# Kernel optimization log

Measured on AMD Instinct MI355X. Metric: run time of the kernel, lower is better.

Reference implementation:

```python
import jax, jax.numpy as jnp
import numpy as np

B, L, F = 256, 512, 64
NUM_IDS = 2000
LN_EPS = 1e-5


def setup_inputs() -> dict:
    key = jax.random.key(0)
    ks = jax.random.split(key, 16)
    s = 0.05
    return {
        # padded neighbor-id sequences; 0 is the padding id
        "src_ids": jax.random.randint(ks[0], (B, L), 0, NUM_IDS, dtype=jnp.int64)
        if jax.config.jax_enable_x64 else jax.random.randint(ks[0], (B, L), 0, NUM_IDS, dtype=jnp.int32),
        "dst_ids": jax.random.randint(ks[1], (B, L), 0, NUM_IDS, dtype=jnp.int64)
        if jax.config.jax_enable_x64 else jax.random.randint(ks[1], (B, L), 0, NUM_IDS, dtype=jnp.int32),
        # co-occurrence encode MLP: Linear(1->F), ReLU, Linear(F->F)
        "enc_w1": jax.random.normal(ks[2], (1, F), jnp.float32) * s,
        "enc_b1": jax.random.normal(ks[3], (F,), jnp.float32) * s,
        "enc_w2": jax.random.normal(ks[4], (F, F), jnp.float32) * s,
        "enc_b2": jax.random.normal(ks[5], (F,), jnp.float32) * s,
        # cross-attention projections (bias-free q/k/v as in source)
        "Wq": jax.random.normal(ks[6], (F, F), jnp.float32) * s,
        "Wk": jax.random.normal(ks[7], (F, F), jnp.float32) * s,
        "Wv": jax.random.normal(ks[8], (F, F), jnp.float32) * s,
        "Wo": jax.random.normal(ks[9], (F, F), jnp.float32) * s,
        "bo": jax.random.normal(ks[10], (F,), jnp.float32) * s,
        "ln_g": jnp.ones((F,), jnp.float32),
        "ln_b": jnp.zeros((F,), jnp.float32),
    }


def _counts_in(a, b):
    # for each element of a: how many times does it occur in b (same batch row)
    # equivalent to the np.unique count / mapping-dict lookup in the original
    return (a[:, :, None] == b[:, None, :]).sum(axis=-1).astype(jnp.float32)


def _appearances(a, b):
    # [B, L, 2]: counts of each id of `a` in (a, b); zero out padding (id==0)
    app = jnp.stack([_counts_in(a, a), _counts_in(a, b)], axis=-1)
    return jnp.where((a == 0)[..., None], 0.0, app)


def _encode(app, w1, b1, w2, b2):
    # Linear(1->F) -> ReLU -> Linear(F->F), then sum over the 2 count channels
    h = jax.nn.relu(app[..., None] * w1[0] + b1)  # [B, L, 2, F]
    h = jnp.einsum('blcf,fg->blcg', h, w2) + b2
    return h.sum(axis=2)  # [B, L, F]


def _linear_attn(q, k, v):
    dim = q.shape[-1]
    q = jax.nn.softmax(q, axis=-1) * (dim ** -0.5)
    k = jax.nn.softmax(k, axis=1)  # softmax over sequence dim (dim=-2)
    ctx = jnp.einsum('bld,ble->bde', k, v)
    return jnp.einsum('bld,bde->ble', q, ctx)


def _layer_norm(x, g, b):
    mu = x.mean(axis=-1, keepdims=True)
    var = ((x - mu) ** 2).mean(axis=-1, keepdims=True)
    return (x - mu) * jax.lax.rsqrt(var + LN_EPS) * g + b


def _cross_attn(x, ctx, Wq, Wk, Wv, Wo, bo, ln_g, ln_b):
    q, k, v = x @ Wq, ctx @ Wk, ctx @ Wv
    attn = _linear_attn(q, k, v)
    return _layer_norm(x + attn @ Wo + bo, ln_g, ln_b)


def reference(src_ids, dst_ids, enc_w1, enc_b1, enc_w2, enc_b2,
              Wq, Wk, Wv, Wo, bo, ln_g, ln_b):
    # neighbor co-occurrence counting + encoding
    src_app = _appearances(src_ids, dst_ids)  # [B, L, 2]
    dst_app = _appearances(dst_ids, src_ids)
    src_feat = _encode(src_app, enc_w1, enc_b1, enc_w2, enc_b2)  # [B, L, F]
    dst_feat = _encode(dst_app, enc_w1, enc_b1, enc_w2, enc_b2)
    # linear cross-attention fusion (shared weights, both directions)
    src_out = _cross_attn(src_feat, dst_feat, Wq, Wk, Wv, Wo, bo, ln_g, ln_b)
    dst_out = _cross_attn(dst_feat, src_feat, Wq, Wk, Wv, Wo, bo, ln_g, ln_b)
    return jnp.stack([src_out, dst_out])  # [2, B, L, F]
```

## Files before the change

### kernel.cpp

```cpp
#include <hip/hip_runtime.h>
#include <hip/hip_bf16.h>

#define BB 256
#define LL 512
#define NIDS 2000

typedef float nfloat4 __attribute__((ext_vector_type(4)));

#define WS_TABLE 0

__global__ __launch_bounds__(64) void k_table(
    const float* __restrict__ w1, const float* __restrict__ b1,
    const float* __restrict__ w2, const float* __restrict__ b2,
    float* __restrict__ table) {
  int c = blockIdx.x, f = threadIdx.x;
  __shared__ float h[64];
  h[f] = fmaxf((float)c * w1[f] + b1[f], 0.f);
  __syncthreads();
  float acc = b2[f];
#pragma unroll
  for (int g = 0; g < 64; ++g) acc += h[g] * w2[g * 64 + f];
  table[c * 64 + f] = acc;
}

__global__ __launch_bounds__(256, 3) void k_fused(
    const int* __restrict__ src, const int* __restrict__ dst,
    const float* __restrict__ table,
    const float* __restrict__ Wq, const float* __restrict__ Wk,
    const float* __restrict__ Wv, const float* __restrict__ Wo,
    const float* __restrict__ bo, const float* __restrict__ lng,
    const float* __restrict__ lnb, float* __restrict__ out) {
  __shared__ __align__(16) char smem[50192];
  int*   hist  = (int*)smem;
  float* poolF = (float*)smem;
  int*   hkey  = (int*)(smem + 16384);
  int*   hmult = (int*)(smem + 20480);
  float* fbF   = (float*)(smem + 20480);
  float* Mg    = (float*)(smem + 24576);
  int*   xkey  = (int*)(smem + 41984);
  int*   ckey  = (int*)(smem + 44032);
  int*   cmult = (int*)(smem + 46080);
  int*   pidxl = (int*)(smem + 48128);
  int*   npp   = (int*)(smem + 50176);

  int bd = blockIdx.x, b = bd >> 1, dir = bd & 1;
  int tid = threadIdx.x, tx = tid & 63, ty = tid >> 6;
  int e0 = ty * 16;

  const int* s = src + b * LL;
  const int* d = dst + b * LL;
  int sid0 = s[tid], sid1 = s[tid + 256];
  int did0 = d[tid], did1 = d[tid + 256];
  for (int i = tid; i < 4000; i += 256) hist[i] = 0;
  __syncthreads();
  atomicAdd(&hist[sid0], 1);        atomicAdd(&hist[sid1], 1);
  atomicAdd(&hist[2000 + did0], 1); atomicAdd(&hist[2000 + did1], 1);
  __syncthreads();

  int x0 = dir ? did0 : sid0, x1 = dir ? did1 : sid1;
  int c0 = dir ? sid0 : did0, c1 = dir ? sid1 : did1;
  const int* hx = dir ? hist + 2000 : hist;
  const int* hc = dir ? hist : hist + 2000;

  for (int i = tid; i < 1024; i += 256) { hkey[i] = -1; hmult[i] = 0; }
  if (tid == 0) *npp = 0;
  __syncthreads();
  for (int r = 0; r < 2; ++r) {
    int id = r ? c1 : c0;
    int ca = 0, cb = 0;
    if (id != 0) { ca = hc[id]; cb = hx[id]; }
    int key = ca | (cb << 10);
    int h = (int)(((unsigned)key * 2654435761u) >> 22) & 1023;
    while (true) {
      int old = atomicCAS(&hkey[h], -1, key);
      if (old == -1 || old == key) break;
      h = (h + 1) & 1023;
    }
    atomicAdd(&hmult[h], 1);
  }
  __syncthreads();
  for (int i = tid; i < 1024; i += 256) {
    if (hkey[i] != -1) {
      int idx = atomicAdd(npp, 1);
      ckey[idx]  = hkey[i];
      cmult[idx] = hmult[i];
    }
  }
  __syncthreads();
  int Pc = *npp;
  __syncthreads();

  for (int i = tid; i < 1024; i += 256) { hkey[i] = -1; hmult[i] = 0; }
  if (tid == 0) *npp = 0;
  __syncthreads();
  int slot0, slot1;
  for (int r = 0; r < 2; ++r) {
    int id = r ? x1 : x0;
    int ca = 0, cb = 0;
    if (id != 0) { ca = hx[id]; cb = hc[id]; }
    int key = ca | (cb << 10);
    int h = (int)(((unsigned)key * 2654435761u) >> 22) & 1023;
    while (true) {
      int old = atomicCAS(&hkey[h], -1, key);
      if (old == -1 || old == key) break;
      h = (h + 1) & 1023;
    }
    if (r) slot1 = h; else slot0 = h;
  }
  __syncthreads();
  for (int i = tid; i < 1024; i += 256) {
    int k = hkey[i];
    if (k != -1) {
      int idx = atomicAdd(npp, 1);
      xkey[idx] = k;
      hkey[i] = idx;
    }
  }
  __syncthreads();
  pidxl[tid]       = hkey[slot0];
  pidxl[tid + 256] = hkey[slot1];
  int Px = *npp;
  __syncthreads();

  float* featA = poolF;
  float* pA    = poolF + 1024;
  float* vA    = poolF + 2048;
  float wa[64];
  float macc[16];
#pragma unroll
  for (int e = 0; e < 16; ++e) macc[e] = 0.f;
  float sacc = 0.f;

  for (int j0 = 0; j0 < Pc; j0 += 16) {
    int cN = min(16, Pc - j0);
#pragma unroll
    for (int f = 0; f < 64; ++f) wa[f] = Wk[f * 64 + tx];
    for (int j = ty; j < cN; j += 4) {
      int key = ckey[j0 + j];
      int ca = key & 1023, cb = key >> 10;
      featA[j * 64 + tx] = table[ca * 64 + tx] + table[cb * 64 + tx];
      float kr = 0.f;
      const float4* fb4 = (const float4*)&featA[j * 64];
#pragma unroll
      for (int q = 0; q < 16; ++q) {
        float4 fv = fb4[q];
        kr += fv.x * wa[4 * q] + fv.y * wa[4 * q + 1] + fv.z * wa[4 * q + 2] + fv.w * wa[4 * q + 3];
      }
      float p = __expf(kr) * (float)cmult[j0 + j];
      sacc += p;
      pA[j * 64 + tx] = p;
    }
#pragma unroll
    for (int f = 0; f < 64; ++f) wa[f] = Wv[f * 64 + tx];
    for (int j = ty; j < cN; j += 4) {
      float vr = 0.f;
      const float4* fb4 = (const float4*)&featA[j * 64];
#pragma unroll
      for (int q = 0; q < 16; ++q) {
        float4 fv = fb4[q];
        vr += fv.x * wa[4 * q] + fv.y * wa[4 * q + 1] + fv.z * wa[4 * q + 2] + fv.w * wa[4 * q + 3];
      }
      vA[j * 64 + tx] = vr;
    }
    __syncthreads();
    for (int jj = 0; jj < cN; ++jj) {
      float pg = pA[jj * 64 + tx];
      const float4* vb4 = (const float4*)&vA[jj * 64 + e0];
#pragma unroll
      for (int q = 0; q < 4; ++q) {
        float4 vv = vb4[q];
        macc[4 * q]     += pg * vv.x; macc[4 * q + 1] += pg * vv.y;
        macc[4 * q + 2] += pg * vv.z; macc[4 * q + 3] += pg * vv.w;
      }
    }
    __syncthreads();
  }
  fbF[512 + ty * 64 + tx] = sacc;
  __syncthreads();
  float inv = 1.f / (fbF[512 + tx] + fbF[576 + tx] + fbF[640 + tx] + fbF[704 + tx]);
#pragma unroll
  for (int e = 0; e < 16; ++e) Mg[(e0 + e) * 68 + tx] = macc[e] * inv;
  for (int i = tid; i < 4096; i += 256) poolF[i] = Wo[i];
#pragma unroll
  for (int f = 0; f < 64; ++f) wa[f] = Wq[f * 64 + tx];
  float bov = bo[tx], lg = lng[tx], lb = lnb[tx];
  __syncthreads();

#pragma unroll
  for (int e = 0; e < 16; ++e) macc[e] = 0.f;
  for (int f = 0; f < 64; ++f) {
    float mt = Mg[f * 68 + tx];
    const float4* wo4 = (const float4*)&poolF[f * 64 + e0];
#pragma unroll
    for (int q = 0; q < 4; ++q) {
      float4 w4 = wo4[q];
      macc[4 * q]     += mt * w4.x; macc[4 * q + 1] += mt * w4.y;
      macc[4 * q + 2] += mt * w4.z; macc[4 * q + 3] += mt * w4.w;
    }
  }
  __syncthreads();
#pragma unroll
  for (int e = 0; e < 16; ++e) Mg[(e0 + e) * 68 + tx] = macc[e];
  __syncthreads();

  for (int i0 = 0; i0 < Px; i0 += 64) {
    int cN = min(64, Px - i0);
    for (int jj = ty; jj < cN; jj += 4) {
      int key = xkey[i0 + jj];
      int ca = key & 1023, cb = key >> 10;
      float fv = table[ca * 64 + tx] + table[cb * 64 + tx];
      fbF[ty * 64 + tx] = fv;
      float qr = 0.f;
      const float4* fb4 = (const float4*)&fbF[ty * 64];
#pragma unroll
      for (int q = 0; q < 16; ++q) {
        float4 f4v = fb4[q];
        qr += f4v.x * wa[4 * q] + f4v.y * wa[4 * q + 1] + f4v.z * wa[4 * q + 2] + f4v.w * wa[4 * q + 3];
      }
      float p = __expf(qr);
      float sum = p;
#pragma unroll
      for (int off = 32; off >= 1; off >>= 1) sum += __shfl_xor(sum, off, 64);
      float qh = p / sum * 0.125f;
      fbF[256 + ty * 64 + tx] = qh;
      float at = 0.f;
      const float4* qb4 = (const float4*)&fbF[256 + ty * 64];
      const float4* gt4 = (const float4*)&Mg[tx * 68];
#pragma unroll
      for (int q = 0; q < 16; ++q) {
        float4 qv = qb4[q];
        float4 gv = gt4[q];
        at += qv.x * gv.x + qv.y * gv.y + qv.z * gv.z + qv.w * gv.w;
      }
      float r = fv + at + bov;
      float mu = r;
#pragma unroll
      for (int off = 32; off >= 1; off >>= 1) mu += __shfl_xor(mu, off, 64);
      mu *= (1.f / 64.f);
      float dv = r - mu;
      float var = dv * dv;
#pragma unroll
      for (int off = 32; off >= 1; off >>= 1) var += __shfl_xor(var, off, 64);
      var *= (1.f / 64.f);
      poolF[jj * 64 + tx] = dv * rsqrtf(var + 1e-5f) * lg + lb;
    }
    __syncthreads();
    const nfloat4* w4 = (const nfloat4*)poolF;
    nfloat4* out4 = (nfloat4*)(out + (size_t)(dir * BB + b) * (LL * 64));
    for (int idx = tid; idx < 512 * 16; idx += 256) {
      int l = idx >> 4, q = idx & 15;
      int pid = pidxl[l];
      if (pid >= i0 && pid < i0 + cN)
        __builtin_nontemporal_store(w4[(pid - i0) * 16 + q], &out4[l * 16 + q]);
    }
    __syncthreads();
  }
}

extern "C" void kernel_launch(void* const* d_in, const int* in_sizes, int n_in,
                              void* d_out, int out_size, void* d_ws, size_t ws_size,
                              hipStream_t stream) {
  const int* src  = (const int*)d_in[0];
  const int* dst  = (const int*)d_in[1];
  const float* w1 = (const float*)d_in[2];
  const float* b1 = (const float*)d_in[3];
  const float* w2 = (const float*)d_in[4];
  const float* b2 = (const float*)d_in[5];
  const float* Wq = (const float*)d_in[6];
  const float* Wk = (const float*)d_in[7];
  const float* Wv = (const float*)d_in[8];
  const float* Wo = (const float*)d_in[9];
  const float* bo = (const float*)d_in[10];
  const float* lng = (const float*)d_in[11];
  const float* lnb = (const float*)d_in[12];
  float* out = (float*)d_out;
  float* table = (float*)d_ws + WS_TABLE;

  k_table<<<dim3(513), dim3(64), 0, stream>>>(w1, b1, w2, b2, table);
  k_fused<<<dim3(512), dim3(256), 0, stream>>>(src, dst, table,
                                               Wq, Wk, Wv, Wo, bo, lng, lnb, out);
}
```

Baseline: 129.8 us.

## Fuse encode-table computation into main kernel with per-block compacted LDS table

Drops the separate k_table launch. Each block now collects the distinct count values used by its keys, computes encoded feature rows only for those values into shared memory, and remaps keys to local indices. Feature gathers then read LDS instead of a global table, and one kernel launch is saved. In exchange each block redoes the MLP work for its own values, and shared memory grows to about 76KB with occupancy lowered to 2 blocks.

```diff
diff --git a/kernel.cpp b/kernel.cpp
--- a/kernel.cpp
+++ b/kernel.cpp
@@ -3,45 +3,32 @@
 
 #define BB 256
 #define LL 512
-#define NIDS 2000
 
 typedef float nfloat4 __attribute__((ext_vector_type(4)));
 
-#define WS_TABLE 0
-
-__global__ __launch_bounds__(64) void k_table(
+__global__ __launch_bounds__(256, 2) void k_all(
+    const int* __restrict__ src, const int* __restrict__ dst,
     const float* __restrict__ w1, const float* __restrict__ b1,
     const float* __restrict__ w2, const float* __restrict__ b2,
-    float* __restrict__ table) {
-  int c = blockIdx.x, f = threadIdx.x;
-  __shared__ float h[64];
-  h[f] = fmaxf((float)c * w1[f] + b1[f], 0.f);
-  __syncthreads();
-  float acc = b2[f];
-#pragma unroll
-  for (int g = 0; g < 64; ++g) acc += h[g] * w2[g * 64 + f];
-  table[c * 64 + f] = acc;
-}
-
-__global__ __launch_bounds__(256, 3) void k_fused(
-    const int* __restrict__ src, const int* __restrict__ dst,
-    const float* __restrict__ table,
     const float* __restrict__ Wq, const float* __restrict__ Wk,
     const float* __restrict__ Wv, const float* __restrict__ Wo,
     const float* __restrict__ bo, const float* __restrict__ lng,
     const float* __restrict__ lnb, float* __restrict__ out) {
-  __shared__ __align__(16) char smem[50192];
+  __shared__ __align__(16) char smem[77840];
   int*   hist  = (int*)smem;
   float* poolF = (float*)smem;
   int*   hkey  = (int*)(smem + 16384);
   int*   hmult = (int*)(smem + 20480);
-  float* fbF   = (float*)(smem + 20480);
-  float* Mg    = (float*)(smem + 24576);
-  int*   xkey  = (int*)(smem + 41984);
-  int*   ckey  = (int*)(smem + 44032);
-  int*   cmult = (int*)(smem + 46080);
-  int*   pidxl = (int*)(smem + 48128);
-  int*   npp   = (int*)(smem + 50176);
+  float* tabL  = (float*)(smem + 16384);
+  int*   cflag = (int*)(smem + 49152);
+  int*   clist = (int*)(smem + 51252);
+  float* Mg    = (float*)(smem + 49152);
+  int*   xkey  = (int*)(smem + 66560);
+  int*   ckey  = (int*)(smem + 68608);
+  int*   cmult = (int*)(smem + 70656);
+  int*   pidxl = (int*)(smem + 72704);
+  float* fbF   = (float*)(smem + 74752);
+  int*   npp   = (int*)(smem + 77824);
 
   int bd = blockIdx.x, b = bd >> 1, dir = bd & 1;
   int tid = threadIdx.x, tx = tid & 63, ty = tid >> 6;
@@ -90,7 +77,7 @@
   int Pc = *npp;
   __syncthreads();
 
-  for (int i = tid; i < 1024; i += 256) { hkey[i] = -1; hmult[i] = 0; }
+  for (int i = tid; i < 1024; i += 256) { hkey[i] = -1; }
   if (tid == 0) *npp = 0;
   __syncthreads();
   int slot0, slot1;
@@ -122,10 +109,48 @@
   int Px = *npp;
   __syncthreads();
 
+  for (int i = tid; i < 513; i += 256) cflag[i] = 0;
+  if (tid == 0) *npp = 0;
+  __syncthreads();
+  if (tid < Pc) { int k = ckey[tid]; cflag[k & 1023] = 1; cflag[k >> 10] = 1; }
+  if (tid < Px) { int k = xkey[tid]; cflag[k & 1023] = 1; cflag[k >> 10] = 1; }
+  __syncthreads();
+  for (int c = tid; c < 513; c += 256) {
+    if (cflag[c]) {
+      int idx = atomicAdd(npp, 1);
+      clist[idx] = c;
+      cflag[c] = idx;
+    }
+  }
+  __syncthreads();
+  int nc = *npp;
+  if (tid < Pc) { int k = ckey[tid]; ckey[tid] = cflag[k & 1023] | (cflag[k >> 10] << 10); }
+  if (tid < Px) { int k = xkey[tid]; xkey[tid] = cflag[k & 1023] | (cflag[k >> 10] << 10); }
+  __syncthreads();
+
+  float wa[64];
+#pragma unroll
+  for (int f = 0; f < 64; ++f) wa[f] = w2[f * 64 + tx];
+  {
+    float w1v = w1[tx], b1v = b1[tx], b2v = b2[tx];
+    for (int i = ty; i < nc; i += 4) {
+      float c = (float)clist[i];
+      poolF[ty * 64 + tx] = fmaxf(c * w1v + b1v, 0.f);
+      float acc = b2v;
+      const float4* h4 = (const float4*)&poolF[ty * 64];
+#pragma unroll
+      for (int q = 0; q < 16; ++q) {
+        float4 hv = h4[q];
+        acc += hv.x * wa[4 * q] + hv.y * wa[4 * q + 1] + hv.z * wa[4 * q + 2] + hv.w * wa[4 * q + 3];
+      }
+      tabL[i * 64 + tx] = acc;
+    }
+  }
+  __syncthreads();
+
   float* featA = poolF;
   float* pA    = poolF + 1024;
   float* vA    = poolF + 2048;
-  float wa[64];
   float macc[16];
 #pragma unroll
   for (int e = 0; e < 16; ++e) macc[e] = 0.f;
@@ -137,8 +162,8 @@
     for (int f = 0; f < 64; ++f) wa[f] = Wk[f * 64 + tx];
     for (int j = ty; j < cN; j += 4) {
       int key = ckey[j0 + j];
-      int ca = key & 1023, cb = key >> 10;
-      featA[j * 64 + tx] = table[ca * 64 + tx] + table[cb * 64 + tx];
+      int ia = key & 1023, ib = key >> 10;
+      featA[j * 64 + tx] = tabL[ia * 64 + tx] + tabL[ib * 64 + tx];
       float kr = 0.f;
       const float4* fb4 = (const float4*)&featA[j * 64];
 #pragma unroll
@@ -207,8 +232,8 @@
     int cN = min(64, Px - i0);
     for (int jj = ty; jj < cN; jj += 4) {
       int key = xkey[i0 + jj];
-      int ca = key & 1023, cb = key >> 10;
-      float fv = table[ca * 64 + tx] + table[cb * 64 + tx];
+      int ia = key & 1023, ib = key >> 10;
+      float fv = tabL[ia * 64 + tx] + tabL[ib * 64 + tx];
       fbF[ty * 64 + tx] = fv;
       float qr = 0.f;
       const float4* fb4 = (const float4*)&fbF[ty * 64];
@@ -274,9 +299,7 @@
   const float* lng = (const float*)d_in[11];
   const float* lnb = (const float*)d_in[12];
   float* out = (float*)d_out;
-  float* table = (float*)d_ws + WS_TABLE;
-
-  k_table<<<dim3(513), dim3(64), 0, stream>>>(w1, b1, w2, b2, table);
-  k_fused<<<dim3(512), dim3(256), 0, stream>>>(src, dst, table,
-                                               Wq, Wk, Wv, Wo, bo, lng, lnb, out);
+
+  k_all<<<dim3(512), dim3(256), 0, stream>>>(src, dst, w1, b1, w2, b2,
+                                             Wq, Wk, Wv, Wo, bo, lng, lnb, out);
 }
```

Result: faster. 120.7 us (-7.0%).
